# Optimization experiments

Hardware: AMD Instinct MI355X
Metric: run time of the kernel (lower is better)

## Reference

```python
import jax, jax.numpy as jnp
import numpy as np

N = 40000   # nodes
E = 640000  # edges (before self-loops)
G = 64      # graphs
EPS = 1e-5


def _gat_conv(x, src, dst, W, a_src, a_dst, bias, n_nodes):
    """PyG GATConv, heads=1, leaky_relu slope 0.2, with self-loops already in src/dst."""
    h = x @ W.T                              # [N, out]
    s_score = h @ a_src                      # [N]
    d_score = h @ a_dst                      # [N]
    e = jax.nn.leaky_relu(s_score[src] + d_score[dst], 0.2)  # [E]
    m = jax.ops.segment_max(e, dst, num_segments=n_nodes)
    ex = jnp.exp(e - m[dst])
    z = jax.ops.segment_sum(ex, dst, num_segments=n_nodes)
    alpha = ex / z[dst]                      # per-dst softmax over incoming edges
    out = jax.ops.segment_sum(h[src] * alpha[:, None], dst, num_segments=n_nodes)
    return out + bias


def _layer_norm(x, gamma, beta):
    mu = jnp.mean(x, axis=-1, keepdims=True)
    var = jnp.mean((x - mu) ** 2, axis=-1, keepdims=True)
    return gamma * (x - mu) * jax.lax.rsqrt(var + EPS) + beta


def setup_inputs() -> dict:
    key = jax.random.key(0)
    ks = jax.random.split(key, 16)
    x = jax.random.normal(ks[0], (N, 128), dtype=jnp.float32)
    edge_index = jax.random.randint(ks[1], (2, E), 0, N, dtype=jnp.int32)
    batch = jnp.sort(jax.random.randint(ks[2], (N,), 0, G, dtype=jnp.int32))
    def glorot(k, shape):
        fan = shape[-1]
        return jax.random.normal(k, shape, dtype=jnp.float32) / jnp.sqrt(jnp.float32(fan))
    return {
        "x": x, "edge_index": edge_index, "batch": batch,
        "W1": glorot(ks[3], (128, 128)), "a1_src": glorot(ks[4], (128,)),
        "a1_dst": glorot(ks[5], (128,)), "b1": jnp.zeros((128,), jnp.float32),
        "g1": jnp.ones((128,), jnp.float32), "be1": jnp.zeros((128,), jnp.float32),
        "W2": glorot(ks[6], (64, 128)), "a2_src": glorot(ks[7], (64,)),
        "a2_dst": glorot(ks[8], (64,)), "b2": jnp.zeros((64,), jnp.float32),
        "g2": jnp.ones((64,), jnp.float32), "be2": jnp.zeros((64,), jnp.float32),
        "Wl": glorot(ks[9], (64, 64)), "bl": jnp.zeros((64,), jnp.float32),
        "Wc": glorot(ks[10], (1, 64)), "bc": jnp.zeros((1,), jnp.float32),
    }


def reference(x, edge_index, batch, W1, a1_src, a1_dst, b1, g1, be1,
              W2, a2_src, a2_dst, b2, g2, be2, Wl, bl, Wc, bc):
    # add self-loops as PyG GATConv does by default
    loops = jnp.arange(N, dtype=edge_index.dtype)
    src = jnp.concatenate([edge_index[0], loops])
    dst = jnp.concatenate([edge_index[1], loops])

    h = jax.nn.relu(_gat_conv(x, src, dst, W1, a1_src, a1_dst, b1, N))
    h = _layer_norm(h, g1, be1)
    h = jax.nn.relu(_gat_conv(h, src, dst, W2, a2_src, a2_dst, b2, N))
    h = _layer_norm(h, g2, be2)

    # global mean pool over graphs
    sums = jax.ops.segment_sum(h, batch, num_segments=G)          # [G, 64]
    cnt = jax.ops.segment_sum(jnp.ones((N,), h.dtype), batch, num_segments=G)
    pooled = sums / jnp.maximum(cnt, 1.0)[:, None]

    out = pooled @ Wl.T + bl
    out = out @ Wc.T + bc                                          # [G, 1]
    return out.squeeze(-1)                                         # [G]
```

## Files before the change

kernel.cpp:

```cpp
#include <hip/hip_runtime.h>
#include <hip/hip_fp16.h>
#include <math.h>

#define NNODES 40000
#define NEDGES 640000
#define NGRAPH 64
#define CAP 96
#define BIN_BLOCKS ((NEDGES + 255) / 256)
constexpr float LN_EPS = 1e-5f;

typedef _Float16 half2_t __attribute__((ext_vector_type(2)));

#if defined(__has_builtin)
#if __has_builtin(__builtin_amdgcn_fdot2)
#define HAS_FDOT2 1
#endif
#endif

__device__ __forceinline__ float dot2acc(half2_t x, half2_t w, float acc) {
#ifdef HAS_FDOT2
    return __builtin_amdgcn_fdot2(x, w, acc, false);
#else
    return acc + (float)x.x * (float)w.x + (float)x.y * (float)w.y;
#endif
}

__device__ __forceinline__ float bf_sum(float v) {
    #pragma unroll
    for (int o = 32; o > 0; o >>= 1) v += __shfl_xor(v, o);
    return v;
}

__global__ void prep(const float* __restrict__ W1, const float* __restrict__ W2,
                     unsigned* __restrict__ Wth1, unsigned* __restrict__ Wth2,
                     int* __restrict__ cnt, float* __restrict__ sums) {
    int t = blockIdx.x * 256 + threadIdx.x;
    if (t < NNODES) cnt[t] = 0;
    if (t < 64 * 128) {
        int i2 = t / 128, o = t % 128;
        half2_t h = { (_Float16)W1[o * 128 + 2 * i2], (_Float16)W1[o * 128 + 2 * i2 + 1] };
        Wth1[i2 * 128 + o] = __builtin_bit_cast(unsigned, h);
    }
    if (t < 64 * 64) {
        int i2 = t / 64, o = t % 64;
        half2_t h = { (_Float16)W2[o * 128 + 2 * i2], (_Float16)W2[o * 128 + 2 * i2 + 1] };
        Wth2[i2 * 64 + o] = __builtin_bit_cast(unsigned, h);
    }
    if (t < NGRAPH * 64) sums[t] = 0.f;
}

template<int DIN, int DOUT, int NPT>
__device__ __forceinline__ void gemm_body(
        int gb, const float* __restrict__ X, const unsigned* __restrict__ Wth,
        const float* __restrict__ asrc, const float* __restrict__ adst,
        __half* __restrict__ H, float* __restrict__ S, float* __restrict__ Dv,
        unsigned* xsu ,
        float* psf   ) {
    constexpr int CHG = DOUT / 4;
    constexpr int NG  = 256 / CHG;
    constexpr int NPB = 64;
    constexpr int K2  = DIN / 2;
    static_assert(NG * NPT == NPB, "grid math");
    const int base = gb * NPB;
    const int tid = threadIdx.x;
    #pragma unroll
    for (int i4 = tid; i4 < NPB * DIN / 4; i4 += 256) {
        const int nd = i4 % NPB, c4 = i4 / NPB;
        float4 v = *(const float4*)(X + (size_t)(base + nd) * DIN + 4 * c4);
        half2_t a = { (_Float16)v.x, (_Float16)v.y };
        half2_t b = { (_Float16)v.z, (_Float16)v.w };
        xsu[(2 * c4 + 0) * NPB + nd] = __builtin_bit_cast(unsigned, a);
        xsu[(2 * c4 + 1) * NPB + nd] = __builtin_bit_cast(unsigned, b);
    }
    __syncthreads();
    const int cg = tid % CHG, ng = tid / CHG;
    const int c0 = 4 * cg, n0 = ng * NPT;
    float acc[NPT][4];
    #pragma unroll
    for (int n = 0; n < NPT; ++n)
        #pragma unroll
        for (int k = 0; k < 4; ++k) acc[n][k] = 0.f;
    #pragma unroll 2
    for (int i2 = 0; i2 < K2; ++i2) {
        const uint4 wu = *(const uint4*)(Wth + i2 * DOUT + c0);
        half2_t w[4] = { __builtin_bit_cast(half2_t, wu.x), __builtin_bit_cast(half2_t, wu.y),
                         __builtin_bit_cast(half2_t, wu.z), __builtin_bit_cast(half2_t, wu.w) };
        #pragma unroll
        for (int n4 = 0; n4 < NPT / 4; ++n4) {
            const uint4 xu = *(const uint4*)(xsu + i2 * NPB + n0 + 4 * n4);
            half2_t x[4] = { __builtin_bit_cast(half2_t, xu.x), __builtin_bit_cast(half2_t, xu.y),
                             __builtin_bit_cast(half2_t, xu.z), __builtin_bit_cast(half2_t, xu.w) };
            #pragma unroll
            for (int j = 0; j < 4; ++j) {
                const int n = 4 * n4 + j;
                acc[n][0] = dot2acc(x[j], w[0], acc[n][0]);
                acc[n][1] = dot2acc(x[j], w[1], acc[n][1]);
                acc[n][2] = dot2acc(x[j], w[2], acc[n][2]);
                acc[n][3] = dot2acc(x[j], w[3], acc[n][3]);
            }
        }
    }
    #pragma unroll
    for (int n = 0; n < NPT; ++n) {
        half2_t p01 = { (_Float16)acc[n][0], (_Float16)acc[n][1] };
        half2_t p23 = { (_Float16)acc[n][2], (_Float16)acc[n][3] };
        uint2 pk = { __builtin_bit_cast(unsigned, p01), __builtin_bit_cast(unsigned, p23) };
        *(uint2*)(H + (size_t)(base + n0 + n) * DOUT + c0) = pk;
    }
    const float4 asf = *(const float4*)(asrc + c0);
    const float4 adf = *(const float4*)(adst + c0);
    float sp[NPT], dp[NPT];
    #pragma unroll
    for (int n = 0; n < NPT; ++n) {
        sp[n] = acc[n][0]*asf.x + acc[n][1]*asf.y + acc[n][2]*asf.z + acc[n][3]*asf.w;
        dp[n] = acc[n][0]*adf.x + acc[n][1]*adf.y + acc[n][2]*adf.z + acc[n][3]*adf.w;
    }
    #pragma unroll
    for (int o = CHG / 2; o > 0; o >>= 1) {
        #pragma unroll
        for (int n = 0; n < NPT; ++n) {
            sp[n] += __shfl_xor(sp[n], o);
            dp[n] += __shfl_xor(dp[n], o);
        }
    }
    if (cg == 0) {
        #pragma unroll
        for (int n = 0; n < NPT; ++n) {
            psf[(ng * NPT + n) * 2 + 0] = sp[n];
            psf[(ng * NPT + n) * 2 + 1] = dp[n];
        }
    }
    __syncthreads();
    if (tid < NPB) {
        S[base + tid]  = psf[tid * 2 + 0];
        Dv[base + tid] = psf[tid * 2 + 1];
    }
}

__global__ __launch_bounds__(256) void bin_gemm1(
        const int* __restrict__ ei,
        int* __restrict__ cnt, unsigned short* __restrict__ ssrc,
        const float* __restrict__ X, const unsigned* __restrict__ Wth1,
        const float* __restrict__ a1s, const float* __restrict__ a1d,
        __half* __restrict__ H, float* __restrict__ S, float* __restrict__ Dv) {
    __shared__ unsigned xsu[64 * 64];
    __shared__ float psf[64 * 2];
    if (blockIdx.x < BIN_BLOCKS) {
        int e = blockIdx.x * 256 + threadIdx.x;
        if (e < NEDGES) {
            int s = ei[e], d = ei[NEDGES + e];
            int pos = atomicAdd(cnt + d, 1);
            if (pos < CAP) ssrc[d * CAP + pos] = (unsigned short)s;
        }
    } else {
        gemm_body<128, 128, 8>(blockIdx.x - BIN_BLOCKS, X, Wth1, a1s, a1d,
                               H, S, Dv, xsu, psf);
    }
}

__global__ __launch_bounds__(256) void gemm2_k(
        const float* __restrict__ X, const unsigned* __restrict__ Wth2,
        const float* __restrict__ a2s, const float* __restrict__ a2d,
        __half* __restrict__ H, float* __restrict__ S, float* __restrict__ Dv) {
    __shared__ unsigned xsu[64 * 64];
    __shared__ float psf[64 * 2];
    gemm_body<128, 64, 4>(blockIdx.x, X, Wth2, a2s, a2d, H, S, Dv, xsu, psf);
}

template<int D, int POOL>
__global__ __launch_bounds__(256) void gat_aggr(
        const int* __restrict__ cnt, const unsigned short* __restrict__ ssrc,
        const float* __restrict__ S, const float* __restrict__ Dv,
        const __half* __restrict__ H,
        const float* __restrict__ b, const float* __restrict__ gam,
        const float* __restrict__ bet,
        float* __restrict__ out, const int* __restrict__ batch,
        float* __restrict__ sums) {
    constexpr int VPL = D / 64;
    const int lane = threadIdx.x & 63;
    const int node = blockIdx.x * 4 + (threadIdx.x >> 6);
    const int deg = min(__builtin_amdgcn_readfirstlane(cnt[node]), CAP);
    const float dsc = Dv[node];
    float ts = S[node] + dsc;
    ts = ts > 0.f ? ts : 0.2f * ts;
    const float aself = __expf(ts);

    float z, acc0 = 0.f, acc1 = 0.f;

    if (deg <= 64) {
        int s = 0; float a = 0.f;
        if (lane < deg) {
            s = ssrc[node * CAP + lane];
            float t = S[s] + dsc;
            t = t > 0.f ? t : 0.2f * t;
            a = __expf(t);
        }
        z = bf_sum(a);
        const int ab = __float_as_int(a);
        const int nmax = (deg + 7) & ~7;
        for (int j = 0; j < nmax; j += 8) {
            float af[8]; __half2 hv[8]; __half hs[8];
            #pragma unroll
            for (int u = 0; u < 8; ++u) {
                const int sj = __builtin_amdgcn_readlane(s, j + u);
                af[u] = __int_as_float(__builtin_amdgcn_readlane(ab, j + u));
                const __half* hp = H + (size_t)sj * D;
                if (VPL == 1) hs[u] = hp[lane];
                else          hv[u] = *(const __half2*)(hp + 2 * lane);
            }
            #pragma unroll
            for (int u = 0; u < 8; ++u) {
                if (VPL == 1) {
                    acc0 += af[u] * __half2float(hs[u]);
                } else {
                    acc0 += af[u] * __half2float(__low2half(hv[u]));
                    acc1 += af[u] * __half2float(__high2half(hv[u]));
                }
            }
        }
    } else {
        float zz = 0.f;
        const int r0 = node * CAP;
        for (int bse = 0; bse < deg; bse += 64) {
            const int n = min(64, deg - bse);
            int s = 0; float a = 0.f;
            if (lane < n) {
                s = ssrc[r0 + bse + lane];
                float t = S[s] + dsc;
                t = t > 0.f ? t : 0.2f * t;
                a = __expf(t);
            }
            zz += bf_sum(a);
            const int abits = __float_as_int(a);
            for (int j = 0; j < n; ++j) {
                const int sj = __builtin_amdgcn_readlane(s, j);
                const float aj = __int_as_float(__builtin_amdgcn_readlane(abits, j));
                const __half* hp = H + (size_t)sj * D;
                if (VPL == 1) {
                    acc0 += aj * __half2float(hp[lane]);
                } else {
                    const float2 f = __half22float2(*(const __half2*)(hp + 2 * lane));
                    acc0 += aj * f.x; acc1 += aj * f.y;
                }
            }
        }
        z = zz;
    }

    {
        const __half* hp = H + (size_t)node * D;
        if (VPL == 1) {
            acc0 += aself * __half2float(hp[lane]);
        } else {
            const float2 f = __half22float2(*(const __half2*)(hp + 2 * lane));
            acc0 += aself * f.x; acc1 += aself * f.y;
        }
        z += aself;
    }

    const float zinv = 1.0f / z;
    float vv[VPL], lsum = 0.f;
    vv[0] = acc0;
    if (VPL == 2) vv[1] = acc1;
    #pragma unroll
    for (int k = 0; k < VPL; ++k) {
        const int ch = VPL * lane + k;
        vv[k] = fmaxf(vv[k] * zinv + b[ch], 0.f);
        lsum += vv[k];
    }
    const float mu = bf_sum(lsum) / D;
    float q = 0.f;
    #pragma unroll
    for (int k = 0; k < VPL; ++k) { vv[k] -= mu; q += vv[k] * vv[k]; }
    const float rstd = rsqrtf(bf_sum(q) / D + LN_EPS);
    #pragma unroll
    for (int k = 0; k < VPL; ++k) {
        const int ch = VPL * lane + k;
        vv[k] = gam[ch] * vv[k] * rstd + bet[ch];
    }
    if (POOL) {
        const int bg = batch[node];
        atomicAdd(&sums[bg * D + lane], vv[0]);
    } else {
        if (VPL == 1) out[(size_t)node * D + lane] = vv[0];
        else *(float2*)(out + (size_t)node * D + 2 * lane) = make_float2(vv[0], vv[1]);
    }
}

__global__ void final_head(const float* __restrict__ sums, const int* __restrict__ batch,
                           const float* __restrict__ Wl, const float* __restrict__ bl,
                           const float* __restrict__ Wc, const float* __restrict__ bc,
                           float* __restrict__ out) {
    __shared__ float p[64];
    __shared__ float red[64];
    const int g = blockIdx.x, tid = threadIdx.x;
    int lo = 0, hi = NNODES;
    while (lo < hi) { int mid = (lo + hi) >> 1; if (batch[mid] < g) lo = mid + 1; else hi = mid; }
    int lo2 = lo, hi2 = NNODES;
    while (lo2 < hi2) { int mid = (lo2 + hi2) >> 1; if (batch[mid] < g + 1) lo2 = mid + 1; else hi2 = mid; }
    const float cnt = (float)(lo2 - lo);
    p[tid] = sums[g * 64 + tid] / fmaxf(cnt, 1.0f);
    __syncthreads();
    float t = bl[tid];
    #pragma unroll 8
    for (int k = 0; k < 64; ++k) t += Wl[tid * 64 + k] * p[k];
    red[tid] = Wc[tid] * t;
    __syncthreads();
    for (int s = 32; s > 0; s >>= 1) {
        if (tid < s) red[tid] += red[tid + s];
        __syncthreads();
    }
    if (tid == 0) out[g] = red[0] + bc[0];
}

extern "C" void kernel_launch(void* const* d_in, const int* in_sizes, int n_in,
                              void* d_out, int out_size, void* d_ws, size_t ws_size,
                              hipStream_t stream) {
    const int N = NNODES, G = NGRAPH;

    const float* x      = (const float*)d_in[0];
    const int*   ei     = (const int*)d_in[1];
    const int*   batch  = (const int*)d_in[2];
    const float* W1     = (const float*)d_in[3];
    const float* a1s    = (const float*)d_in[4];
    const float* a1d    = (const float*)d_in[5];
    const float* b1     = (const float*)d_in[6];
    const float* g1     = (const float*)d_in[7];
    const float* be1    = (const float*)d_in[8];
    const float* W2     = (const float*)d_in[9];
    const float* a2s    = (const float*)d_in[10];
    const float* a2d    = (const float*)d_in[11];
    const float* b2     = (const float*)d_in[12];
    const float* g2     = (const float*)d_in[13];
    const float* be2    = (const float*)d_in[14];
    const float* Wl     = (const float*)d_in[15];
    const float* bl     = (const float*)d_in[16];
    const float* Wc     = (const float*)d_in[17];
    const float* bc     = (const float*)d_in[18];

    char* w = (char*)d_ws;
    __half* h1  = (__half*)w; w += (size_t)N * 128 * 2;
    float* acc1 = (float*)w; w += (size_t)N * 128 * 4;
    float* S    = (float*)w; w += (size_t)N * 4;
    float* Dv   = (float*)w; w += (size_t)N * 4;
    int* cnt    = (int*)w;   w += (size_t)N * 4;
    unsigned short* ssrc = (unsigned short*)w; w += (size_t)N * CAP * 2;
    unsigned* Wth1 = (unsigned*)w; w += (size_t)64 * 128 * 4;
    unsigned* Wth2 = (unsigned*)w; w += (size_t)64 * 64 * 4;
    float* sums = (float*)w; w += (size_t)G * 64 * 4;
    __half* h2 = h1;

    const int gridN = (N + 255) / 256;

    prep<<<gridN, 256, 0, stream>>>(W1, W2, Wth1, Wth2, cnt, sums);

    bin_gemm1<<<BIN_BLOCKS + N / 64, 256, 0, stream>>>(
        ei, cnt, ssrc, x, Wth1, a1s, a1d, h1, S, Dv);

    gat_aggr<128, 0><<<N / 4, 256, 0, stream>>>(cnt, ssrc, S, Dv, h1, b1, g1, be1,
                                                acc1, nullptr, nullptr);

    gemm2_k<<<N / 64, 256, 0, stream>>>(acc1, Wth2, a2s, a2d, h2, S, Dv);
    gat_aggr<64, 1><<<N / 4, 256, 0, stream>>>(cnt, ssrc, S, Dv, h2, b2, g2, be2,
                                               nullptr, batch, sums);

    final_head<<<G, 64, 0, stream>>>(sums, batch, Wl, bl, Wc, bc, (float*)d_out);
}
```

Before: 279.2 us.

## Fuse all stages into one cooperative persistent kernel with grid syncs

Replaces the six separate kernel launches with a single cooperative kernel. It runs persistent blocks over each stage's work and uses grid.sync between stages, aiming to remove per-launch overhead and inter-kernel gaps. The head is rewritten to do one graph per wavefront using shuffles. The change risks lower occupancy and load imbalance from grid-stride loops over a limited resident grid, plus the cost of the grid barriers. It falls back to the multi-kernel path if the cooperative launch fails.

Result: slower. 643.5 us (+130.5%).

```diff
diff --git a/kernel.cpp b/kernel.cpp
--- a/kernel.cpp
+++ b/kernel.cpp
@@ -1,12 +1,16 @@
 #include <hip/hip_runtime.h>
+#include <hip/hip_cooperative_groups.h>
 #include <hip/hip_fp16.h>
 #include <math.h>
+
+namespace cg = cooperative_groups;
 
 #define NNODES 40000
 #define NEDGES 640000
 #define NGRAPH 64
 #define CAP 96
-#define BIN_BLOCKS ((NEDGES + 255) / 256)
+#define NT1 (NNODES / 64)
+#define BINC ((NEDGES + 255) / 256)
 constexpr float LN_EPS = 1e-5f;
 
 typedef _Float16 half2_t __attribute__((ext_vector_type(2)));
@@ -31,31 +35,12 @@
     return v;
 }
 
-__global__ void prep(const float* __restrict__ W1, const float* __restrict__ W2,
-                     unsigned* __restrict__ Wth1, unsigned* __restrict__ Wth2,
-                     int* __restrict__ cnt, float* __restrict__ sums) {
-    int t = blockIdx.x * 256 + threadIdx.x;
-    if (t < NNODES) cnt[t] = 0;
-    if (t < 64 * 128) {
-        int i2 = t / 128, o = t % 128;
-        half2_t h = { (_Float16)W1[o * 128 + 2 * i2], (_Float16)W1[o * 128 + 2 * i2 + 1] };
-        Wth1[i2 * 128 + o] = __builtin_bit_cast(unsigned, h);
-    }
-    if (t < 64 * 64) {
-        int i2 = t / 64, o = t % 64;
-        half2_t h = { (_Float16)W2[o * 128 + 2 * i2], (_Float16)W2[o * 128 + 2 * i2 + 1] };
-        Wth2[i2 * 64 + o] = __builtin_bit_cast(unsigned, h);
-    }
-    if (t < NGRAPH * 64) sums[t] = 0.f;
-}
-
 template<int DIN, int DOUT, int NPT>
 __device__ __forceinline__ void gemm_body(
         int gb, const float* __restrict__ X, const unsigned* __restrict__ Wth,
         const float* __restrict__ asrc, const float* __restrict__ adst,
         __half* __restrict__ H, float* __restrict__ S, float* __restrict__ Dv,
-        unsigned* xsu ,
-        float* psf   ) {
+        unsigned* xsu, float* psf) {
     constexpr int CHG = DOUT / 4;
     constexpr int NG  = 256 / CHG;
     constexpr int NPB = 64;
@@ -73,8 +58,8 @@
         xsu[(2 * c4 + 1) * NPB + nd] = __builtin_bit_cast(unsigned, b);
     }
     __syncthreads();
-    const int cg = tid % CHG, ng = tid / CHG;
-    const int c0 = 4 * cg, n0 = ng * NPT;
+    const int cg_ = tid % CHG, ng = tid / CHG;
+    const int c0 = 4 * cg_, n0 = ng * NPT;
     float acc[NPT][4];
     #pragma unroll
     for (int n = 0; n < NPT; ++n)
@@ -123,7 +108,7 @@
             dp[n] += __shfl_xor(dp[n], o);
         }
     }
-    if (cg == 0) {
+    if (cg_ == 0) {
         #pragma unroll
         for (int n = 0; n < NPT; ++n) {
             psf[(ng * NPT + n) * 2 + 0] = sp[n];
@@ -135,41 +120,12 @@
         S[base + tid]  = psf[tid * 2 + 0];
         Dv[base + tid] = psf[tid * 2 + 1];
     }
-}
-
-__global__ __launch_bounds__(256) void bin_gemm1(
-        const int* __restrict__ ei,
-        int* __restrict__ cnt, unsigned short* __restrict__ ssrc,
-        const float* __restrict__ X, const unsigned* __restrict__ Wth1,
-        const float* __restrict__ a1s, const float* __restrict__ a1d,
-        __half* __restrict__ H, float* __restrict__ S, float* __restrict__ Dv) {
-    __shared__ unsigned xsu[64 * 64];
-    __shared__ float psf[64 * 2];
-    if (blockIdx.x < BIN_BLOCKS) {
-        int e = blockIdx.x * 256 + threadIdx.x;
-        if (e < NEDGES) {
-            int s = ei[e], d = ei[NEDGES + e];
-            int pos = atomicAdd(cnt + d, 1);
-            if (pos < CAP) ssrc[d * CAP + pos] = (unsigned short)s;
-        }
-    } else {
-        gemm_body<128, 128, 8>(blockIdx.x - BIN_BLOCKS, X, Wth1, a1s, a1d,
-                               H, S, Dv, xsu, psf);
-    }
-}
-
-__global__ __launch_bounds__(256) void gemm2_k(
-        const float* __restrict__ X, const unsigned* __restrict__ Wth2,
-        const float* __restrict__ a2s, const float* __restrict__ a2d,
-        __half* __restrict__ H, float* __restrict__ S, float* __restrict__ Dv) {
-    __shared__ unsigned xsu[64 * 64];
-    __shared__ float psf[64 * 2];
-    gemm_body<128, 64, 4>(blockIdx.x, X, Wth2, a2s, a2d, H, S, Dv, xsu, psf);
+    __syncthreads();
 }
 
 template<int D, int POOL>
-__global__ __launch_bounds__(256) void gat_aggr(
-        const int* __restrict__ cnt, const unsigned short* __restrict__ ssrc,
+__device__ __forceinline__ void gat_body(
+        int nb, const int* __restrict__ cnt, const unsigned short* __restrict__ ssrc,
         const float* __restrict__ S, const float* __restrict__ Dv,
         const __half* __restrict__ H,
         const float* __restrict__ b, const float* __restrict__ gam,
@@ -178,7 +134,7 @@
         float* __restrict__ sums) {
     constexpr int VPL = D / 64;
     const int lane = threadIdx.x & 63;
-    const int node = blockIdx.x * 4 + (threadIdx.x >> 6);
+    const int node = nb * 4 + (threadIdx.x >> 6);
     const int deg = min(__builtin_amdgcn_readfirstlane(cnt[node]), CAP);
     const float dsc = Dv[node];
     float ts = S[node] + dsc;
@@ -287,56 +243,139 @@
     }
 }
 
-__global__ void final_head(const float* __restrict__ sums, const int* __restrict__ batch,
-                           const float* __restrict__ Wl, const float* __restrict__ bl,
-                           const float* __restrict__ Wc, const float* __restrict__ bc,
-                           float* __restrict__ out) {
-    __shared__ float p[64];
-    __shared__ float red[64];
-    const int g = blockIdx.x, tid = threadIdx.x;
+__device__ __forceinline__ void prep_body(
+        int t, const float* __restrict__ W1, const float* __restrict__ W2,
+        unsigned* __restrict__ Wth1, unsigned* __restrict__ Wth2,
+        int* __restrict__ cnt, float* __restrict__ sums) {
+    if (t < NNODES) cnt[t] = 0;
+    if (t < 64 * 128) {
+        int i2 = t / 128, o = t % 128;
+        half2_t h = { (_Float16)W1[o * 128 + 2 * i2], (_Float16)W1[o * 128 + 2 * i2 + 1] };
+        Wth1[i2 * 128 + o] = __builtin_bit_cast(unsigned, h);
+    }
+    if (t < 64 * 64) {
+        int i2 = t / 64, o = t % 64;
+        half2_t h = { (_Float16)W2[o * 128 + 2 * i2], (_Float16)W2[o * 128 + 2 * i2 + 1] };
+        Wth2[i2 * 64 + o] = __builtin_bit_cast(unsigned, h);
+    }
+    if (t < NGRAPH * 64) sums[t] = 0.f;
+}
+
+__device__ __forceinline__ void head_body(
+        int g, int lane, const float* __restrict__ sums, const int* __restrict__ batch,
+        const float* __restrict__ Wl, const float* __restrict__ bl,
+        const float* __restrict__ Wc, const float* __restrict__ bc,
+        float* __restrict__ out) {
     int lo = 0, hi = NNODES;
-    while (lo < hi) { int mid = (lo + hi) >> 1; if (batch[mid] < g) lo = mid + 1; else hi = mid; }
+    while (lo < hi) { int m = (lo + hi) >> 1; if (batch[m] < g) lo = m + 1; else hi = m; }
     int lo2 = lo, hi2 = NNODES;
-    while (lo2 < hi2) { int mid = (lo2 + hi2) >> 1; if (batch[mid] < g + 1) lo2 = mid + 1; else hi2 = mid; }
-    const float cnt = (float)(lo2 - lo);
-    p[tid] = sums[g * 64 + tid] / fmaxf(cnt, 1.0f);
-    __syncthreads();
-    float t = bl[tid];
+    while (lo2 < hi2) { int m = (lo2 + hi2) >> 1; if (batch[m] < g + 1) lo2 = m + 1; else hi2 = m; }
+    const float c = (float)(lo2 - lo);
+    const float pv = sums[g * 64 + lane] / fmaxf(c, 1.0f);
+    float t = bl[lane];
     #pragma unroll 8
-    for (int k = 0; k < 64; ++k) t += Wl[tid * 64 + k] * p[k];
-    red[tid] = Wc[tid] * t;
-    __syncthreads();
-    for (int s = 32; s > 0; s >>= 1) {
-        if (tid < s) red[tid] += red[tid + s];
-        __syncthreads();
-    }
-    if (tid == 0) out[g] = red[0] + bc[0];
+    for (int k = 0; k < 64; ++k) t += Wl[lane * 64 + k] * __shfl(pv, k);
+    const float r = bf_sum(Wc[lane] * t);
+    if (lane == 0) out[g] = r + bc[0];
+}
+
+struct P {
+    const int *ei, *batch;
+    const float *x, *W1, *a1s, *a1d, *b1, *g1, *be1;
+    const float *W2, *a2s, *a2d, *b2, *g2, *be2;
+    const float *Wl, *bl, *Wc, *bc;
+    __half* h; float* acc1; float* S; float* Dv;
+    int* cnt; unsigned short* ssrc;
+    unsigned *Wth1, *Wth2; float* sums; float* out;
+};
+
+__global__ __launch_bounds__(256) void mega(P p) {
+    __shared__ unsigned xsu[64 * 64];
+    __shared__ float psf[128];
+    cg::grid_group grid = cg::this_grid();
+    const int tid = threadIdx.x;
+    const int GR = gridDim.x;
+
+    for (int t = blockIdx.x * 256 + tid; t < NNODES; t += GR * 256)
+        prep_body(t, p.W1, p.W2, p.Wth1, p.Wth2, p.cnt, p.sums);
+    grid.sync();
+
+    for (int w = blockIdx.x; w < NT1 + BINC; w += GR) {
+        if (w < NT1) {
+            gemm_body<128, 128, 8>(w, p.x, p.Wth1, p.a1s, p.a1d, p.h, p.S, p.Dv, xsu, psf);
+        } else {
+            int e = (w - NT1) * 256 + tid;
+            if (e < NEDGES) {
+                int s = p.ei[e], d = p.ei[NEDGES + e];
+                int pos = atomicAdd(p.cnt + d, 1);
+                if (pos < CAP) p.ssrc[d * CAP + pos] = (unsigned short)s;
+            }
+        }
+    }
+    grid.sync();
+
+    for (int nb = blockIdx.x; nb < NNODES / 4; nb += GR)
+        gat_body<128, 0>(nb, p.cnt, p.ssrc, p.S, p.Dv, p.h,
+                         p.b1, p.g1, p.be1, p.acc1, nullptr, nullptr);
+    grid.sync();
+
+    for (int w = blockIdx.x; w < NT1; w += GR)
+        gemm_body<128, 64, 4>(w, p.acc1, p.Wth2, p.a2s, p.a2d, p.h, p.S, p.Dv, xsu, psf);
+    grid.sync();
+
+    for (int nb = blockIdx.x; nb < NNODES / 4; nb += GR)
+        gat_body<64, 1>(nb, p.cnt, p.ssrc, p.S, p.Dv, p.h,
+                        p.b2, p.g2, p.be2, nullptr, p.batch, p.sums);
+    grid.sync();
+
+    {
+        const int g = blockIdx.x * 4 + (tid >> 6);
+        if (g < NGRAPH)
+            head_body(g, tid & 63, p.sums, p.batch, p.Wl, p.bl, p.Wc, p.bc, p.out);
+    }
+}
+
+__global__ __launch_bounds__(256) void prep_k(P p) {
+    prep_body(blockIdx.x * 256 + threadIdx.x, p.W1, p.W2, p.Wth1, p.Wth2, p.cnt, p.sums);
+}
+__global__ __launch_bounds__(256) void bin_gemm1_k(P p) {
+    __shared__ unsigned xsu[64 * 64];
+    __shared__ float psf[128];
+    if (blockIdx.x < BINC) {
+        int e = blockIdx.x * 256 + threadIdx.x;
+        if (e < NEDGES) {
+            int s = p.ei[e], d = p.ei[NEDGES + e];
+            int pos = atomicAdd(p.cnt + d, 1);
+            if (pos < CAP) p.ssrc[d * CAP + pos] = (unsigned short)s;
+        }
+    } else {
+        gemm_body<128, 128, 8>(blockIdx.x - BINC, p.x, p.Wth1, p.a1s, p.a1d,
+                               p.h, p.S, p.Dv, xsu, psf);
+    }
+}
+__global__ __launch_bounds__(256) void gat1_k(P p) {
+    gat_body<128, 0>(blockIdx.x, p.cnt, p.ssrc, p.S, p.Dv, p.h,
+                     p.b1, p.g1, p.be1, p.acc1, nullptr, nullptr);
+}
+__global__ __launch_bounds__(256) void gemm2_k(P p) {
+    __shared__ unsigned xsu[64 * 64];
+    __shared__ float psf[128];
+    gemm_body<128, 64, 4>(blockIdx.x, p.acc1, p.Wth2, p.a2s, p.a2d, p.h, p.S, p.Dv, xsu, psf);
+}
+__global__ __launch_bounds__(256) void gat2_k(P p) {
+    gat_body<64, 1>(blockIdx.x, p.cnt, p.ssrc, p.S, p.Dv, p.h,
+                    p.b2, p.g2, p.be2, nullptr, p.batch, p.sums);
+}
+__global__ void head_k(P p) {
+    const int g = blockIdx.x * 4 + (threadIdx.x >> 6);
+    if (g < NGRAPH)
+        head_body(g, threadIdx.x & 63, p.sums, p.batch, p.Wl, p.bl, p.Wc, p.bc, p.out);
 }
 
 extern "C" void kernel_launch(void* const* d_in, const int* in_sizes, int n_in,
                               void* d_out, int out_size, void* d_ws, size_t ws_size,
                               hipStream_t stream) {
     const int N = NNODES, G = NGRAPH;
-
-    const float* x      = (const float*)d_in[0];
-    const int*   ei     = (const int*)d_in[1];
-    const int*   batch  = (const int*)d_in[2];
-    const float* W1     = (const float*)d_in[3];
-    const float* a1s    = (const float*)d_in[4];
-    const float* a1d    = (const float*)d_in[5];
-    const float* b1     = (const float*)d_in[6];
-    const float* g1     = (const float*)d_in[7];
-    const float* be1    = (const float*)d_in[8];
-    const float* W2     = (const float*)d_in[9];
-    const float* a2s    = (const float*)d_in[10];
-    const float* a2d    = (const float*)d_in[11];
-    const float* b2     = (const float*)d_in[12];
-    const float* g2     = (const float*)d_in[13];
-    const float* be2    = (const float*)d_in[14];
-    const float* Wl     = (const float*)d_in[15];
-    const float* bl     = (const float*)d_in[16];
-    const float* Wc     = (const float*)d_in[17];
-    const float* bc     = (const float*)d_in[18];
 
     char* w = (char*)d_ws;
     __half* h1  = (__half*)w; w += (size_t)N * 128 * 2;
@@ -348,21 +387,50 @@
     unsigned* Wth1 = (unsigned*)w; w += (size_t)64 * 128 * 4;
     unsigned* Wth2 = (unsigned*)w; w += (size_t)64 * 64 * 4;
     float* sums = (float*)w; w += (size_t)G * 64 * 4;
-    __half* h2 = h1;
-
-    const int gridN = (N + 255) / 256;
-
-    prep<<<gridN, 256, 0, stream>>>(W1, W2, Wth1, Wth2, cnt, sums);
-
-    bin_gemm1<<<BIN_BLOCKS + N / 64, 256, 0, stream>>>(
-        ei, cnt, ssrc, x, Wth1, a1s, a1d, h1, S, Dv);
-
-    gat_aggr<128, 0><<<N / 4, 256, 0, stream>>>(cnt, ssrc, S, Dv, h1, b1, g1, be1,
-                                                acc1, nullptr, nullptr);
-
-    gemm2_k<<<N / 64, 256, 0, stream>>>(acc1, Wth2, a2s, a2d, h2, S, Dv);
-    gat_aggr<64, 1><<<N / 4, 256, 0, stream>>>(cnt, ssrc, S, Dv, h2, b2, g2, be2,
-                                               nullptr, batch, sums);
-
-    final_head<<<G, 64, 0, stream>>>(sums, batch, Wl, bl, Wc, bc, (float*)d_out);
-}
+
+    P prm;
+    prm.ei   = (const int*)d_in[1];
+    prm.batch= (const int*)d_in[2];
+    prm.x    = (const float*)d_in[0];
+    prm.W1   = (const float*)d_in[3];
+    prm.a1s  = (const float*)d_in[4];
+    prm.a1d  = (const float*)d_in[5];
+    prm.b1   = (const float*)d_in[6];
+    prm.g1   = (const float*)d_in[7];
+    prm.be1  = (const float*)d_in[8];
+    prm.W2   = (const float*)d_in[9];
+    prm.a2s  = (const float*)d_in[10];
+    prm.a2d  = (const float*)d_in[11];
+    prm.b2   = (const float*)d_in[12];
+    prm.g2   = (const float*)d_in[13];
+    prm.be2  = (const float*)d_in[14];
+    prm.Wl   = (const float*)d_in[15];
+    prm.bl   = (const float*)d_in[16];
+    prm.Wc   = (const float*)d_in[17];
+    prm.bc   = (const float*)d_in[18];
+    prm.h = h1; prm.acc1 = acc1; prm.S = S; prm.Dv = Dv;
+    prm.cnt = cnt; prm.ssrc = ssrc; prm.Wth1 = Wth1; prm.Wth2 = Wth2;
+    prm.sums = sums; prm.out = (float*)d_out;
+
+    int nbpc = 0, ncu = 0;
+    hipError_t e1 = hipOccupancyMaxActiveBlocksPerMultiprocessor(
+                        &nbpc, (const void*)mega, 256, 0);
+    hipError_t e2 = hipDeviceGetAttribute(&ncu, hipDeviceAttributeMultiprocessorCount, 0);
+    int grid = (e1 == hipSuccess && e2 == hipSuccess) ? nbpc * ncu : 0;
+
+    hipError_t lerr = hipErrorUnknown;
+    if (grid >= 64) {
+        void* kargs[] = { &prm };
+        lerr = hipLaunchCooperativeKernel((void*)mega, dim3(grid), dim3(256),
+                                          kargs, 0, stream);
+    }
+    if (lerr != hipSuccess) {
+        const int gridN = (N + 255) / 256;
+        prep_k<<<gridN, 256, 0, stream>>>(prm);
+        bin_gemm1_k<<<BINC + NT1, 256, 0, stream>>>(prm);
+        gat1_k<<<N / 4, 256, 0, stream>>>(prm);
+        gemm2_k<<<NT1, 256, 0, stream>>>(prm);
+        gat2_k<<<N / 4, 256, 0, stream>>>(prm);
+        head_k<<<16, 256, 0, stream>>>(prm);
+    }
+}
```
